# Optimization experiments

Measured on AMD Instinct MI355X. Metric: run time of the kernel, lower is better.

## Reference

```python
import jax, jax.numpy as jnp
import numpy as np

N, M, E, IN, HID = 100000, 2048, 65536, 512, 256
TAU, LAMDA = 0.5, 1.0


def _l2n(a, eps=1e-12):
    # F.normalize: x / max(||x||_2, eps) along dim=1
    return a / jnp.maximum(jnp.linalg.norm(a, axis=1, keepdims=True), eps)


def setup_inputs() -> dict:
    key = jax.random.key(0)
    ks = jax.random.split(key, 16)
    s = 0.05  # weight scale (xavier-like)
    inp = {
        "x": jax.random.normal(ks[0], (N, IN), jnp.float32),
        "We0": jax.random.normal(ks[1], (IN, HID), jnp.float32) * s,
        "be0": jnp.zeros((HID,), jnp.float32),
        "We1": jax.random.normal(ks[2], (HID, HID), jnp.float32) * s,
        "be1": jnp.zeros((HID,), jnp.float32),
        "Wt0": jax.random.normal(ks[3], (IN, HID), jnp.float32) * s,
        "bt0": jnp.zeros((HID,), jnp.float32),
        "Wt1": jax.random.normal(ks[4], (HID, HID), jnp.float32) * s,
        "bt1": jnp.zeros((HID,), jnp.float32),
        "Wp0": jax.random.normal(ks[5], (HID, HID), jnp.float32) * s,
        "bp0": jnp.zeros((HID,), jnp.float32),
        "Wp1": jax.random.normal(ks[6], (HID, HID), jnp.float32) * s,
        "bp1": jnp.zeros((HID,), jnp.float32),
        "p_vals": jnp.ones((N,), jnp.float32),
        "cg_vals": jax.random.uniform(ks[7], (E,), jnp.float32),
        "p_assign": jax.random.randint(ks[8], (N,), 0, M, jnp.int32),
        "cg_rows": jax.random.randint(ks[9], (E,), 0, M, jnp.int32),
        "cg_cols": jax.random.randint(ks[10], (E,), 0, M, jnp.int32),
        "neg_idx": jax.random.randint(ks[11], (N,), 0, M, jnp.int32),
    }
    return inp


def reference(x, We0, be0, We1, be1, Wt0, bt0, Wt1, bt1,
              Wp0, bp0, Wp1, bp1, p_vals, cg_vals,
              p_assign, cg_rows, cg_cols, neg_idx):
    # encoder: stacked Linears, no activation (batch_norm=layer_norm=False)
    h = (x @ We0 + be0) @ We1 + be1                      # [N, HID]
    # h = spmm(P.T, h): per-cluster weighted sum
    hc = jax.ops.segment_sum(p_vals[:, None] * h, p_assign, num_segments=M)  # [M, HID]
    # target encoder
    v = (x @ Wt0 + bt0) @ Wt1 + bt1                      # [N, HID]

    # pos_score: projector (relu between layers, none on last) + normalize
    q = jax.nn.relu(hc @ Wp0 + bp0) @ Wp1 + bp1          # [M, HID]
    q = _l2n(q)
    vn = _l2n(v)
    pos_sim = jnp.sum(vn * q[p_assign], axis=1) / TAU    # [N]
    pos_score = jnp.exp(
        jax.ops.segment_sum(p_vals * pos_sim, p_assign, num_segments=M))[:, None]  # [M,1]

    # neg_score: dense cluster-cluster similarity
    hn = _l2n(hc)
    neg_score = jnp.exp((hn @ hn.T) / TAU)               # [M, M]

    # partition_score = coarse_g @ neg_score (sparse row-scatter)
    partition_score = jax.ops.segment_sum(
        cg_vals[:, None] * neg_score[cg_cols], cg_rows, num_segments=M)  # [M, M]

    loss = jnp.mean(-jnp.log(pos_score + LAMDA * partition_score)
                    + jnp.log(pos_score + neg_score.sum(axis=1)))
    return loss
```

## Files before the change

kernel.cpp:

```cpp
#include <hip/hip_runtime.h>
#include <hip/hip_bf16.h>
#include <math.h>

#define N_PTS  100000
#define M_CL   2048
#define E_EDG  65536
#define IN_DIM 512
#define HID    256

typedef unsigned short u16;
typedef __attribute__((ext_vector_type(8))) short bf16x8;
typedef __attribute__((ext_vector_type(4))) float f32x4;

__device__ __forceinline__ u16 f2bf(float f){
  __hip_bfloat16 h = __float2bfloat16(f);
  return *reinterpret_cast<u16*>(&h);
}
__device__ __forceinline__ unsigned pk2(float a, float b){
  return (unsigned)f2bf(a) | ((unsigned)f2bf(b) << 16);
}
__device__ __forceinline__ float bf2f(u16 v){
  return __uint_as_float((unsigned)v << 16);
}
__device__ __forceinline__ void glds16(const u16* g, u16* lds_base_uniform){
  __builtin_amdgcn_global_load_lds(
      (const __attribute__((address_space(1))) unsigned int*)(g),
      (__attribute__((address_space(3))) unsigned int*)(lds_base_uniform), 16, 0, 0);
}
#define VMWAIT8() do{ asm volatile("s_waitcnt vmcnt(8)" ::: "memory"); __builtin_amdgcn_sched_barrier(0);}while(0)
#define VMWAIT4() do{ asm volatile("s_waitcnt vmcnt(4)" ::: "memory"); __builtin_amdgcn_sched_barrier(0);}while(0)
#define VMWAIT0() do{ asm volatile("s_waitcnt vmcnt(0)" ::: "memory"); __builtin_amdgcn_sched_barrier(0);}while(0)

static const size_t OFF_POSACC = 0;
static const size_t OFF_NEGSUM = 8192;
static const size_t OFF_CURP   = 16384;
static const size_t OFF_CURE   = 24576;
static const size_t OFF_LOSS   = 32768;
static const size_t OFF_DONE   = 32776;
static const size_t OFF_STARTP = 33024;
static const size_t OFF_STARTE = 41472;
static const size_t OFF_SORTPT = 49920;
static const size_t OFF_SCOL   = 450048;
static const size_t OFF_SVAL   = 712192;
static const size_t OFF_CNT    = 974336;
static const size_t OFF_XC     = 982528;
static const size_t OFF_Q      = 9371136;
static const size_t OFF_HNB    = 11468288;
static const size_t OFF_NEGB   = 13565440;
static const size_t OFF_WT0T   = 22020096;
static const size_t OFF_WT1T   = 22282240;
static const size_t OFF_XBF    = 33554432;

__global__ __launch_bounds__(1024) void k_setup(
    const int* __restrict__ pas, const int* __restrict__ cgr,
    int* __restrict__ start_p, int* __restrict__ start_e,
    int* __restrict__ cur_p, int* __restrict__ cur_e,
    float* __restrict__ posacc, float* __restrict__ negsum,
    double* __restrict__ lossd, int* __restrict__ done){
  __shared__ int hist[2048];
  __shared__ int wpart[16];
  const int t = threadIdx.x;
  const int lane = t & 63, wv = t >> 6;

  posacc[2*t] = 0.f; posacc[2*t+1] = 0.f;
  negsum[2*t] = 0.f; negsum[2*t+1] = 0.f;
  cur_p[2*t] = 0;    cur_p[2*t+1] = 0;
  cur_e[2*t] = 0;    cur_e[2*t+1] = 0;
  if (t == 0){ *lossd = 0.0; *done = 0; }
  hist[2*t] = 0; hist[2*t+1] = 0;
  __syncthreads();

  for (int i=t; i<N_PTS; i+=1024) atomicAdd(&hist[pas[i]], 1);
  __syncthreads();
  {
    int v0 = hist[2*t], v1 = hist[2*t+1];
    int s = v0 + v1;
    for (int off=1; off<64; off<<=1){ int n = __shfl_up(s, off, 64); if (lane >= off) s += n; }
    if (lane == 63) wpart[wv] = s;
    __syncthreads();
    if (t == 0){ int run = 0; for (int i=0;i<16;i++){ int tmp = wpart[i]; wpart[i] = run; run += tmp; } }
    __syncthreads();
    int excl = s - (v0+v1) + wpart[wv];
    start_p[2*t] = excl; start_p[2*t+1] = excl + v0;
    if (t == 1023) start_p[2048] = excl + v0 + v1;
  }
  __syncthreads();
  hist[2*t] = 0; hist[2*t+1] = 0;
  __syncthreads();
  for (int i=t; i<E_EDG; i+=1024) atomicAdd(&hist[cgr[i]], 1);
  __syncthreads();
  {
    int v0 = hist[2*t], v1 = hist[2*t+1];
    int s = v0 + v1;
    for (int off=1; off<64; off<<=1){ int n = __shfl_up(s, off, 64); if (lane >= off) s += n; }
    if (lane == 63) wpart[wv] = s;
    __syncthreads();
    if (t == 0){ int run = 0; for (int i=0;i<16;i++){ int tmp = wpart[i]; wpart[i] = run; run += tmp; } }
    __syncthreads();
    int excl = s - (v0+v1) + wpart[wv];
    start_e[2*t] = excl; start_e[2*t+1] = excl + v0;
    if (t == 1023) start_e[2048] = excl + v0 + v1;
  }
}

#define NB_P  ((N_PTS + 255)/256)
#define NB_E  ((E_EDG + 255)/256)
#define NB_T0 ((256*512)/256)
#define NB_T1 ((256*256)/256)
__global__ __launch_bounds__(256) void k_misc(
    const int* __restrict__ pas, const int* __restrict__ cgr, const int* __restrict__ cgc,
    const float* __restrict__ cgv, const int* __restrict__ start_p, const int* __restrict__ start_e,
    int* __restrict__ cur_p, int* __restrict__ cur_e,
    int* __restrict__ sortpt, int* __restrict__ scol, float* __restrict__ sval,
    const float* __restrict__ Wt0, const float* __restrict__ Wt1,
    u16* __restrict__ Wt0t, u16* __restrict__ Wt1t){
  const int b = blockIdx.x, t = threadIdx.x;
  if (b < NB_P){
    int i = b*256 + t;
    if (i < N_PTS){
      int r = pas[i];
      int p = start_p[r] + atomicAdd(&cur_p[r], 1);
      sortpt[p] = i;
    }
  } else if (b < NB_P + NB_E){
    int e = (b - NB_P)*256 + t;
    if (e < E_EDG){
      int r = cgr[e];
      int p = start_e[r] + atomicAdd(&cur_e[r], 1);
      scol[p] = cgc[e];
      sval[p] = cgv[e];
    }
  } else if (b < NB_P + NB_E + NB_T0){
    int o = (b - NB_P - NB_E)*256 + t;
    int n = o / IN_DIM, k = o % IN_DIM;
    Wt0t[o] = f2bf(Wt0[(size_t)k*HID + n]);
  } else {
    int o = (b - NB_P - NB_E - NB_T0)*256 + t;
    int n = o / HID, k = o % HID;
    Wt1t[o] = f2bf(Wt1[(size_t)k*HID + n]);
  }
}

__global__ __launch_bounds__(256) void k_cluster_agg(const float* __restrict__ x, const float* __restrict__ pv,
                                                     const int* __restrict__ sorted_pt, const int* __restrict__ start,
                                                     float* __restrict__ Xc, float* __restrict__ cnt,
                                                     u16* __restrict__ xbf){
  const int m = blockIdx.x;
  const int t = threadIdx.x;
  const int half = t >> 7;
  const int u = t & 127;
  const int s0 = start[m], s1 = start[m+1];
  f32x4 a = {0.f,0.f,0.f,0.f};
  float c = 0.f;
  for (int p = s0 + half; p < s1; p += 2){
    int row = sorted_pt[p];
    float w = pv[row];
    f32x4 xv = *reinterpret_cast<const f32x4*>(x + (size_t)row*IN_DIM + u*4);
    a.x = fmaf(w, xv.x, a.x); a.y = fmaf(w, xv.y, a.y);
    a.z = fmaf(w, xv.z, a.z); a.w = fmaf(w, xv.w, a.w);
    c += w;
    uint2 pk; pk.x = pk2(xv.x, xv.y); pk.y = pk2(xv.z, xv.w);
    *reinterpret_cast<uint2*>(xbf + (size_t)row*IN_DIM + u*4) = pk;
  }
  __shared__ __align__(16) float sh[128*4];
  __shared__ float shc[2];
  if (half == 1) *reinterpret_cast<f32x4*>(sh + u*4) = a;
  if (t == 0)   shc[0] = c;
  if (t == 128) shc[1] = c;
  __syncthreads();
  if (half == 0){
    f32x4 b = *reinterpret_cast<const f32x4*>(sh + u*4);
    a.x += b.x; a.y += b.y; a.z += b.z; a.w += b.w;
    *reinterpret_cast<f32x4*>(Xc + (size_t)m*IN_DIM + u*4) = a;
    if (t == 0) cnt[m] = shc[0] + shc[1];
  }
}

template<int K>
__device__ __forceinline__ void mc_layer(const float* __restrict__ W, const float* act, int t, float acc[4]){
#pragma unroll
  for (int r=0;r<4;r++) acc[r] = 0.f;
#pragma unroll 2
  for (int k=0;k<K;k+=4){
    float w0 = W[(size_t)(k+0)*HID + t];
    float w1 = W[(size_t)(k+1)*HID + t];
    float w2 = W[(size_t)(k+2)*HID + t];
    float w3 = W[(size_t)(k+3)*HID + t];
#pragma unroll
    for (int r=0;r<4;r++){
      float4 av = *reinterpret_cast<const float4*>(act + r*K + k);
      acc[r] = fmaf(av.x, w0, acc[r]);
      acc[r] = fmaf(av.y, w1, acc[r]);
      acc[r] = fmaf(av.z, w2, acc[r]);
      acc[r] = fmaf(av.w, w3, acc[r]);
    }
  }
}

__global__ __launch_bounds__(256) void k_mchain(
    const float* __restrict__ Xc, const float* __restrict__ cnt,
    const float* __restrict__ We0, const float* __restrict__ be0,
    const float* __restrict__ We1, const float* __restrict__ be1,
    const float* __restrict__ Wp0, const float* __restrict__ bp0,
    const float* __restrict__ Wp1, const float* __restrict__ bp1,
    u16* __restrict__ hnb, float* __restrict__ q){
  __shared__ __align__(16) float a_sh[4*512];
  __shared__ __align__(16) float b_sh[4*256];
  __shared__ float part[4][4];
  const int t = threadIdx.x;
  const int rb = blockIdx.x*4;
  for (int i=t; i<4*128; i+=256){
    int r = i>>7, k4 = i&127;
    reinterpret_cast<float4*>(a_sh + r*512)[k4] =
      reinterpret_cast<const float4*>(Xc + (size_t)(rb+r)*IN_DIM)[k4];
  }
  float cv[4];
#pragma unroll
  for (int r=0;r<4;r++) cv[r] = cnt[rb+r];
  __syncthreads();

  float acc[4], v[4];
  mc_layer<512>(We0, a_sh, t, acc);
  {
    float b = be0[t];
#pragma unroll
    for (int r=0;r<4;r++) b_sh[r*256+t] = fmaf(cv[r], b, acc[r]);
  }
  __syncthreads();
  mc_layer<256>(We1, b_sh, t, acc);
  {
    float b = be1[t];
#pragma unroll
    for (int r=0;r<4;r++){
      v[r] = fmaf(cv[r], b, acc[r]);
      float s = v[r]*v[r];
#pragma unroll
      for (int off=32;off;off>>=1) s += __shfl_xor(s, off, 64);
      if ((t&63) == 0) part[t>>6][r] = s;
      a_sh[r*256+t] = v[r];
    }
  }
  __syncthreads();
#pragma unroll
  for (int r=0;r<4;r++){
    float tot = part[0][r]+part[1][r]+part[2][r]+part[3][r];
    float inv = 1.0f / fmaxf(sqrtf(tot), 1e-12f);
    hnb[(size_t)(rb+r)*HID + t] = f2bf(v[r]*inv);
  }
  mc_layer<256>(Wp0, a_sh, t, acc);
  {
    float b = bp0[t];
#pragma unroll
    for (int r=0;r<4;r++) b_sh[r*256+t] = fmaxf(acc[r]+b, 0.f);
  }
  __syncthreads();
  mc_layer<256>(Wp1, b_sh, t, acc);
  {
    float b = bp1[t];
#pragma unroll
    for (int r=0;r<4;r++){
      v[r] = acc[r] + b;
      float s = v[r]*v[r];
#pragma unroll
      for (int off=32;off;off>>=1) s += __shfl_xor(s, off, 64);
      if ((t&63) == 0) part[t>>6][r] = s;
    }
  }
  __syncthreads();
#pragma unroll
  for (int r=0;r<4;r++){
    float tot = part[0][r]+part[1][r]+part[2][r]+part[3][r];
    float inv = 1.0f / fmaxf(sqrtf(tot), 1e-12f);
    q[(size_t)(rb+r)*HID + t] = v[r]*inv;
  }
}

#define NEG_BLKS 256
#define TGT_BLKS ((N_PTS + 63)/64)
__global__ __launch_bounds__(256,2) void k_tneg(
    const u16* __restrict__ xbf, const u16* __restrict__ Wt0t, const float* __restrict__ bt0,
    const u16* __restrict__ Wt1t, const float* __restrict__ bt1,
    const float* __restrict__ q, const int* __restrict__ assign,
    const float* __restrict__ pv, float* __restrict__ posacc,
    const u16* __restrict__ hnb, u16* __restrict__ negb, float* __restrict__ negsum){
  __shared__ u16 wlds[4][2][2048];
  __shared__ u16 act[16384];
  __shared__ float red[2][4][4][16];

  const int t  = threadIdx.x;
  const int w  = t >> 6;
  const int l  = t & 63;
  const int c  = l & 15;
  const int lg = l >> 4;
  const int wrow = l >> 2;
  const int wswz = (l&3) ^ ((wrow>>1)&3);
  const int su = lg ^ ((c>>1)&3);

  f32x4 acc[4][4];
#pragma unroll
  for (int i=0;i<4;i++)
#pragma unroll
    for (int j=0;j<4;j++){ acc[i][j].x=0.f; acc[i][j].y=0.f; acc[i][j].z=0.f; acc[i][j].w=0.f; }

  if (blockIdx.x < NEG_BLKS){
    const int b  = blockIdx.x;
    const int j0 = (b & 7) * 256;
    const int i0 = (b >> 3) * 64;

    #define NSTAGE_W(k0, buf) do { \
      _Pragma("unroll") \
      for (int i_=0;i_<4;i_++){ \
        int row_ = j0 + w*64 + i_*16 + wrow; \
        glds16(hnb + (size_t)row_*HID + (k0) + wswz*8, &wlds[w][buf][i_*512]); \
      } } while(0)

    const u16* irow[4];
#pragma unroll
    for (int mf=0;mf<4;mf++)
      irow[mf] = hnb + (size_t)(i0 + mf*16 + c)*HID + lg*8;

    bf16x8 xreg[2][4];
    NSTAGE_W(0, 0);
#pragma unroll
    for (int mf=0;mf<4;mf++) xreg[0][mf] = *reinterpret_cast<const bf16x8*>(irow[mf]);

#pragma unroll
    for (int ks=0; ks<8; ks++){
      const int buf = ks & 1;
      if (ks < 7){
        NSTAGE_W((ks+1)*32, buf^1);
#pragma unroll
        for (int mf=0;mf<4;mf++)
          xreg[buf^1][mf] = *reinterpret_cast<const bf16x8*>(irow[mf] + (ks+1)*32);
        VMWAIT8();
      } else {
        VMWAIT0();
      }
#pragma unroll
      for (int nf=0; nf<4; nf++){
        bf16x8 afr = *reinterpret_cast<const bf16x8*>(&wlds[w][buf][((nf*16+c)*4 + su)*8]);
#pragma unroll
        for (int mf=0; mf<4; mf++)
          acc[mf][nf] = __builtin_amdgcn_mfma_f32_16x16x32_bf16(afr, xreg[buf][mf], acc[mf][nf], 0,0,0);
      }
    }

#pragma unroll
    for (int mf=0; mf<4; mf++){
      int i = i0 + mf*16 + c;
      float rs = 0.f;
#pragma unroll
      for (int nf=0; nf<4; nf++){
        f32x4 a = acc[mf][nf];
        float e0 = __expf(a.x*2.0f), e1 = __expf(a.y*2.0f);
        float e2 = __expf(a.z*2.0f), e3 = __expf(a.w*2.0f);
        rs += e0+e1+e2+e3;
        uint2 p; p.x = pk2(e0, e1); p.y = pk2(e2, e3);
        *reinterpret_cast<uint2*>(negb + (size_t)i*M_CL + j0 + w*64 + nf*16 + lg*4) = p;
      }
      rs += __shfl_xor(rs, 16, 64); rs += __shfl_xor(rs, 32, 64);
      if (lg == 0) atomicAdd(&negsum[i], rs);
    }
    #undef NSTAGE_W
    return;
  }

  const int gm0 = (blockIdx.x - NEG_BLKS) * 64;

  #define TSTAGE_W(Wt, K, k0, buf) do { \
    _Pragma("unroll") \
    for (int i_=0;i_<4;i_++){ \
      int row_ = w*64 + i_*16 + wrow; \
      glds16((Wt) + (size_t)row_*(K) + (k0) + wswz*8, &wlds[w][buf][i_*512]); \
    } } while(0)

  const u16* xrow[4];
#pragma unroll
  for (int mf=0;mf<4;mf++){
    int gm = gm0 + mf*16 + c; if (gm > N_PTS-1) gm = N_PTS-1;
    xrow[mf] = xbf + (size_t)gm*IN_DIM + lg*8;
  }

  bf16x8 xreg[2][4];
  TSTAGE_W(Wt0t, IN_DIM, 0, 0);
#pragma unroll
  for (int mf=0;mf<4;mf++) xreg[0][mf] = *reinterpret_cast<const bf16x8*>(xrow[mf]);

#pragma unroll
  for (int ks=0; ks<16; ks++){
    const int buf = ks & 1;
    if (ks < 15){
      TSTAGE_W(Wt0t, IN_DIM, (ks+1)*32, buf^1);
#pragma unroll
      for (int mf=0;mf<4;mf++)
        xreg[buf^1][mf] = *reinterpret_cast<const bf16x8*>(xrow[mf] + (ks+1)*32);
      VMWAIT8();
    } else {
      VMWAIT0();
    }
#pragma unroll
    for (int nf=0; nf<4; nf++){
      bf16x8 afr = *reinterpret_cast<const bf16x8*>(&wlds[w][buf][((nf*16+c)*4 + su)*8]);
#pragma unroll
      for (int mf=0; mf<4; mf++)
        acc[mf][nf] = __builtin_amdgcn_mfma_f32_16x16x32_bf16(afr, xreg[buf][mf], acc[mf][nf], 0,0,0);
    }
  }

#pragma unroll
  for (int nf=0; nf<4; nf++){
    f32x4 bias = *reinterpret_cast<const f32x4*>(bt0 + w*64 + nf*16 + lg*4);
#pragma unroll
    for (int mf=0; mf<4; mf++){
      int m = mf*16 + c;
      f32x4 v = acc[mf][nf] + bias;
      uint2 p; p.x = pk2(v.x, v.y); p.y = pk2(v.z, v.w);
      int u = (w*8 + nf*2 + (lg>>1)) ^ (c&7);
      *reinterpret_cast<uint2*>(act + (m*32 + u)*8 + (lg&1)*4) = p;
    }
  }
#pragma unroll
  for (int i=0;i<4;i++)
#pragma unroll
    for (int j=0;j<4;j++){ acc[i][j].x=0.f; acc[i][j].y=0.f; acc[i][j].z=0.f; acc[i][j].w=0.f; }
  __syncthreads();

  TSTAGE_W(Wt1t, HID, 0, 0);
#pragma unroll
  for (int ks=0; ks<8; ks++){
    const int buf = ks & 1;
    if (ks < 7){
      TSTAGE_W(Wt1t, HID, (ks+1)*32, buf^1);
      VMWAIT4();
    } else {
      VMWAIT0();
    }
    bf16x8 bfr[4];
#pragma unroll
    for (int mf=0; mf<4; mf++){
      int m = mf*16 + c;
      int u = (ks*4 + lg) ^ (c&7);
      bfr[mf] = *reinterpret_cast<const bf16x8*>(act + (m*32 + u)*8);
    }
#pragma unroll
    for (int nf=0; nf<4; nf++){
      bf16x8 afr = *reinterpret_cast<const bf16x8*>(&wlds[w][buf][((nf*16+c)*4 + su)*8]);
#pragma unroll
      for (int mf=0; mf<4; mf++)
        acc[mf][nf] = __builtin_amdgcn_mfma_f32_16x16x32_bf16(afr, bfr[mf], acc[mf][nf], 0,0,0);
    }
  }

#pragma unroll
  for (int mf=0; mf<4; mf++){
    int gm = gm0 + mf*16 + c;
    int cl = assign[(gm < N_PTS) ? gm : (N_PTS-1)];
    const float* qrow = q + (size_t)cl*HID + w*64 + lg*4;
    float ss = 0.f, d = 0.f;
#pragma unroll
    for (int nf=0; nf<4; nf++){
      f32x4 b  = *reinterpret_cast<const f32x4*>(bt1 + w*64 + nf*16 + lg*4);
      f32x4 qv = *reinterpret_cast<const f32x4*>(qrow + nf*16);
      f32x4 v  = acc[mf][nf] + b;
      ss = fmaf(v.x,v.x, fmaf(v.y,v.y, fmaf(v.z,v.z, fmaf(v.w,v.w, ss))));
      d  = fmaf(v.x,qv.x, fmaf(v.y,qv.y, fmaf(v.z,qv.z, fmaf(v.w,qv.w, d))));
    }
    ss += __shfl_xor(ss, 16, 64); ss += __shfl_xor(ss, 32, 64);
    d  += __shfl_xor(d , 16, 64); d  += __shfl_xor(d , 32, 64);
    if (lg == 0){ red[0][w][mf][c] = ss; red[1][w][mf][c] = d; }
  }
  __syncthreads();
  if (t < 64){
    int gm = gm0 + t;
    if (gm < N_PTS){
      int mf = t>>4, cc = t&15;
      float ss = red[0][0][mf][cc]+red[0][1][mf][cc]+red[0][2][mf][cc]+red[0][3][mf][cc];
      float d  = red[1][0][mf][cc]+red[1][1][mf][cc]+red[1][2][mf][cc]+red[1][3][mf][cc];
      float inv = 1.0f / fmaxf(sqrtf(ss), 1e-12f);
      atomicAdd(&posacc[assign[gm]], pv[gm] * d * inv * 2.0f);
    }
  }
  #undef TSTAGE_W
}

__global__ __launch_bounds__(256) void k_loss(const u16* __restrict__ negb, const float* __restrict__ negsum,
                                              const float* __restrict__ posacc, const int* __restrict__ start,
                                              const int* __restrict__ scol, const float* __restrict__ sval,
                                              double* __restrict__ lossd, int* __restrict__ done,
                                              float* __restrict__ out){
  const int i = blockIdx.x, t = threadIdx.x;
  float ps[8] = {};
  const int s0 = start[i], s1 = start[i+1];
  for (int e=s0;e<s1;e++){
    int c = scol[e];
    float v = sval[e];
    bf16x8 r = *reinterpret_cast<const bf16x8*>(negb + (size_t)c*M_CL + t*8);
#pragma unroll
    for (int jj=0;jj<8;jj++) ps[jj] = fmaf(v, bf2f((u16)r[jj]), ps[jj]);
  }
  float pos = __expf(posacc[i]);
  f32x4 nsa = *reinterpret_cast<const f32x4*>(negsum + t*8);
  f32x4 nsb = *reinterpret_cast<const f32x4*>(negsum + t*8 + 4);
  float ns[8] = {nsa.x,nsa.y,nsa.z,nsa.w,nsb.x,nsb.y,nsb.z,nsb.w};
  float part = 0.f;
#pragma unroll
  for (int jj=0;jj<8;jj++)
    part += __logf(pos + ns[jj]) - __logf(pos + ps[jj]);
#pragma unroll
  for (int off=32;off;off>>=1) part += __shfl_xor(part, off, 64);
  __shared__ float wsum[4];
  if ((t&63) == 0) wsum[t>>6] = part;
  __syncthreads();
  if (t == 0){
    double s = (double)wsum[0] + (double)wsum[1] + (double)wsum[2] + (double)wsum[3];
    atomicAdd(lossd, s);
    __threadfence();
    int ticket = atomicAdd(done, 1);
    if (ticket == M_CL - 1){
      __threadfence();
      double tot = atomicAdd(lossd, 0.0);
      out[0] = (float)(tot / ((double)M_CL * (double)M_CL));
    }
  }
}

extern "C" void kernel_launch(void* const* d_in, const int* in_sizes, int n_in,
                              void* d_out, int out_size, void* d_ws, size_t ws_size,
                              hipStream_t stream){
  const float* x    = (const float*)d_in[0];
  const float* We0  = (const float*)d_in[1];
  const float* be0  = (const float*)d_in[2];
  const float* We1  = (const float*)d_in[3];
  const float* be1  = (const float*)d_in[4];
  const float* Wt0  = (const float*)d_in[5];
  const float* bt0  = (const float*)d_in[6];
  const float* Wt1  = (const float*)d_in[7];
  const float* bt1  = (const float*)d_in[8];
  const float* Wp0  = (const float*)d_in[9];
  const float* bp0  = (const float*)d_in[10];
  const float* Wp1  = (const float*)d_in[11];
  const float* bp1  = (const float*)d_in[12];
  const float* pv   = (const float*)d_in[13];
  const float* cgv  = (const float*)d_in[14];
  const int*   pas  = (const int*)d_in[15];
  const int*   cgr  = (const int*)d_in[16];
  const int*   cgc  = (const int*)d_in[17];

  char* ws = (char*)d_ws;
  float*  posacc  = (float*)(ws + OFF_POSACC);
  float*  negsum  = (float*)(ws + OFF_NEGSUM);
  int*    cur_p   = (int*)  (ws + OFF_CURP);
  int*    cur_e   = (int*)  (ws + OFF_CURE);
  double* lossd   = (double*)(ws + OFF_LOSS);
  int*    done    = (int*)  (ws + OFF_DONE);
  int*    start_p = (int*)  (ws + OFF_STARTP);
  int*    start_e = (int*)  (ws + OFF_STARTE);
  int*    sortpt  = (int*)  (ws + OFF_SORTPT);
  int*    scol    = (int*)  (ws + OFF_SCOL);
  float*  sval    = (float*)(ws + OFF_SVAL);
  float*  cnt     = (float*)(ws + OFF_CNT);
  float*  Xc      = (float*)(ws + OFF_XC);
  float*  qb      = (float*)(ws + OFF_Q);
  u16*    hnb     = (u16*)  (ws + OFF_HNB);
  u16*    negb    = (u16*)  (ws + OFF_NEGB);
  u16*    Wt0t    = (u16*)  (ws + OFF_WT0T);
  u16*    Wt1t    = (u16*)  (ws + OFF_WT1T);
  u16*    xbf     = (u16*)  (ws + OFF_XBF);

  k_setup<<<1, 1024, 0, stream>>>(pas, cgr, start_p, start_e, cur_p, cur_e,
                                  posacc, negsum, lossd, done);

  k_misc<<<NB_P + NB_E + NB_T0 + NB_T1, 256, 0, stream>>>(
      pas, cgr, cgc, cgv, start_p, start_e, cur_p, cur_e,
      sortpt, scol, sval, Wt0, Wt1, Wt0t, Wt1t);

  k_cluster_agg<<<M_CL, 256, 0, stream>>>(x, pv, sortpt, start_p, Xc, cnt, xbf);

  k_mchain<<<M_CL/4, 256, 0, stream>>>(Xc, cnt, We0, be0, We1, be1, Wp0, bp0, Wp1, bp1, hnb, qb);

  k_tneg<<<NEG_BLKS + TGT_BLKS, 256, 0, stream>>>(
      xbf, Wt0t, bt0, Wt1t, bt1, qb, pas, pv, posacc, hnb, negb, negsum);

  k_loss<<<M_CL, 256, 0, stream>>>(negb, negsum, posacc, start_e, scol, sval, lossd, done, (float*)d_out);
}
```

Before: 397.9 us.

## Split target-encoder GEMM chain into weight-stationary persistent kernels and parallelize setup

Replaces the single-block setup kernel with a parallel zeroing kernel, a multi-block histogram kernel and a small scan kernel. Splits the fused target-encoder/negative-score kernel into a separate neg-similarity kernel and three target kernels: a persistent first-layer GEMM that keeps its weight slice resident in LDS and writes a bf16 intermediate to global memory, a persistent second-layer GEMM fused with the dot/norm epilogue writing per-half partials, and a final reduction kernel. The aim is to stop reloading weights per row tile and to remove the serial single-block setup, at the cost of an extra global round-trip for the hidden activations and more kernel launches.

```diff
diff --git a/kernel.cpp b/kernel.cpp
--- a/kernel.cpp
+++ b/kernel.cpp
@@ -27,80 +27,77 @@
       (const __attribute__((address_space(1))) unsigned int*)(g),
       (__attribute__((address_space(3))) unsigned int*)(lds_base_uniform), 16, 0, 0);
 }
+#define VMWAIT0() do{ asm volatile("s_waitcnt vmcnt(0)" ::: "memory"); __builtin_amdgcn_sched_barrier(0);}while(0)
 #define VMWAIT8() do{ asm volatile("s_waitcnt vmcnt(8)" ::: "memory"); __builtin_amdgcn_sched_barrier(0);}while(0)
-#define VMWAIT4() do{ asm volatile("s_waitcnt vmcnt(4)" ::: "memory"); __builtin_amdgcn_sched_barrier(0);}while(0)
-#define VMWAIT0() do{ asm volatile("s_waitcnt vmcnt(0)" ::: "memory"); __builtin_amdgcn_sched_barrier(0);}while(0)
 
 static const size_t OFF_POSACC = 0;
 static const size_t OFF_NEGSUM = 8192;
 static const size_t OFF_CURP   = 16384;
 static const size_t OFF_CURE   = 24576;
-static const size_t OFF_LOSS   = 32768;
-static const size_t OFF_DONE   = 32776;
-static const size_t OFF_STARTP = 33024;
-static const size_t OFF_STARTE = 41472;
-static const size_t OFF_SORTPT = 49920;
-static const size_t OFF_SCOL   = 450048;
-static const size_t OFF_SVAL   = 712192;
-static const size_t OFF_CNT    = 974336;
-static const size_t OFF_XC     = 982528;
-static const size_t OFF_Q      = 9371136;
-static const size_t OFF_HNB    = 11468288;
-static const size_t OFF_NEGB   = 13565440;
-static const size_t OFF_WT0T   = 22020096;
-static const size_t OFF_WT1T   = 22282240;
+static const size_t OFF_HISTP  = 32768;
+static const size_t OFF_HISTE  = 40960;
+static const size_t OFF_LOSS   = 49152;
+static const size_t OFF_DONE   = 49160;
+static const int    ZERO_U32   = 12291;
+static const size_t OFF_STARTP = 49664;
+static const size_t OFF_STARTE = 58368;
+static const size_t OFF_SORTPT = 66816;
+static const size_t OFF_SCOL   = 466944;
+static const size_t OFF_SVAL   = 729088;
+static const size_t OFF_CNT    = 991232;
+static const size_t OFF_XC     = 999424;
+static const size_t OFF_Q      = 5193728;
+static const size_t OFF_HNB    = 7290880;
+static const size_t OFF_NEGB   = 8388608;
+static const size_t OFF_WT0T   = 16777216;
+static const size_t OFF_WT1T   = 17039360;
 static const size_t OFF_XBF    = 33554432;
-
-__global__ __launch_bounds__(1024) void k_setup(
-    const int* __restrict__ pas, const int* __restrict__ cgr,
-    int* __restrict__ start_p, int* __restrict__ start_e,
-    int* __restrict__ cur_p, int* __restrict__ cur_e,
-    float* __restrict__ posacc, float* __restrict__ negsum,
-    double* __restrict__ lossd, int* __restrict__ done){
-  __shared__ int hist[2048];
-  __shared__ int wpart[16];
+static const size_t OFF_TBUF   = 150994944;
+static const size_t OFF_PSS    = 260046848;
+static const size_t OFF_PD     = 268435456;
+
+__global__ __launch_bounds__(256) void k_pre0(unsigned* __restrict__ p){
+  int i = blockIdx.x*256 + threadIdx.x;
+  if (i < ZERO_U32) p[i] = 0u;
+}
+
+#define NB_HP ((N_PTS + 255)/256)
+#define NB_HE ((E_EDG + 255)/256)
+__global__ __launch_bounds__(256) void k_hist(const int* __restrict__ pas, const int* __restrict__ cgr,
+                                              int* __restrict__ hist_p, int* __restrict__ hist_e){
+  const int b = blockIdx.x, t = threadIdx.x;
+  if (b < NB_HP){
+    int i = b*256 + t;
+    if (i < N_PTS) atomicAdd(&hist_p[pas[i]], 1);
+  } else {
+    int e = (b - NB_HP)*256 + t;
+    if (e < E_EDG) atomicAdd(&hist_e[cgr[e]], 1);
+  }
+}
+
+__device__ __forceinline__ void scan8(const int* __restrict__ hist, int* __restrict__ start, int* part){
   const int t = threadIdx.x;
-  const int lane = t & 63, wv = t >> 6;
-
-  posacc[2*t] = 0.f; posacc[2*t+1] = 0.f;
-  negsum[2*t] = 0.f; negsum[2*t+1] = 0.f;
-  cur_p[2*t] = 0;    cur_p[2*t+1] = 0;
-  cur_e[2*t] = 0;    cur_e[2*t+1] = 0;
-  if (t == 0){ *lossd = 0.0; *done = 0; }
-  hist[2*t] = 0; hist[2*t+1] = 0;
-  __syncthreads();
-
-  for (int i=t; i<N_PTS; i+=1024) atomicAdd(&hist[pas[i]], 1);
-  __syncthreads();
-  {
-    int v0 = hist[2*t], v1 = hist[2*t+1];
-    int s = v0 + v1;
-    for (int off=1; off<64; off<<=1){ int n = __shfl_up(s, off, 64); if (lane >= off) s += n; }
-    if (lane == 63) wpart[wv] = s;
-    __syncthreads();
-    if (t == 0){ int run = 0; for (int i=0;i<16;i++){ int tmp = wpart[i]; wpart[i] = run; run += tmp; } }
-    __syncthreads();
-    int excl = s - (v0+v1) + wpart[wv];
-    start_p[2*t] = excl; start_p[2*t+1] = excl + v0;
-    if (t == 1023) start_p[2048] = excl + v0 + v1;
-  }
-  __syncthreads();
-  hist[2*t] = 0; hist[2*t+1] = 0;
-  __syncthreads();
-  for (int i=t; i<E_EDG; i+=1024) atomicAdd(&hist[cgr[i]], 1);
-  __syncthreads();
-  {
-    int v0 = hist[2*t], v1 = hist[2*t+1];
-    int s = v0 + v1;
-    for (int off=1; off<64; off<<=1){ int n = __shfl_up(s, off, 64); if (lane >= off) s += n; }
-    if (lane == 63) wpart[wv] = s;
-    __syncthreads();
-    if (t == 0){ int run = 0; for (int i=0;i<16;i++){ int tmp = wpart[i]; wpart[i] = run; run += tmp; } }
-    __syncthreads();
-    int excl = s - (v0+v1) + wpart[wv];
-    start_e[2*t] = excl; start_e[2*t+1] = excl + v0;
-    if (t == 1023) start_e[2048] = excl + v0 + v1;
-  }
+  int v[8]; int s = 0;
+#pragma unroll
+  for (int j=0;j<8;j++){ v[j] = hist[t*8+j]; s += v[j]; }
+  part[t] = s;
+  __syncthreads();
+  if (t == 0){
+    int run = 0;
+    for (int i=0;i<256;i++){ int tmp = part[i]; part[i] = run; run += tmp; }
+  }
+  __syncthreads();
+  int run = part[t];
+#pragma unroll
+  for (int j=0;j<8;j++){ start[t*8+j] = run; run += v[j]; }
+  if (t == 255) start[M_CL] = run;
+}
+__global__ __launch_bounds__(256) void k_scan2(const int* __restrict__ hp, int* __restrict__ sp,
+                                               const int* __restrict__ he, int* __restrict__ se){
+  __shared__ int part[256];
+  scan8(hp, sp, part);
+  __syncthreads();
+  scan8(he, se, part);
 }
 
 #define NB_P  ((N_PTS + 255)/256)
@@ -275,125 +272,212 @@
   }
 }
 
-#define NEG_BLKS 256
-#define TGT_BLKS ((N_PTS + 63)/64)
-__global__ __launch_bounds__(256,2) void k_tneg(
+#define NT0_TILES ((N_PTS + 255)/256)
+__global__ __launch_bounds__(512,2) void k_t0(
     const u16* __restrict__ xbf, const u16* __restrict__ Wt0t, const float* __restrict__ bt0,
-    const u16* __restrict__ Wt1t, const float* __restrict__ bt1,
-    const float* __restrict__ q, const int* __restrict__ assign,
-    const float* __restrict__ pv, float* __restrict__ posacc,
-    const u16* __restrict__ hnb, u16* __restrict__ negb, float* __restrict__ negsum){
-  __shared__ u16 wlds[4][2][2048];
-  __shared__ u16 act[16384];
-  __shared__ float red[2][4][4][16];
-
+    u16* __restrict__ tbuf){
+  __shared__ u16 wbuf[16*64*32];
   const int t  = threadIdx.x;
   const int w  = t >> 6;
   const int l  = t & 63;
   const int c  = l & 15;
   const int lg = l >> 4;
+  const int nq   = blockIdx.x & 3;
+  const int pair = blockIdx.x >> 2;
+  const int nbase = nq*64;
+
+  {
+#pragma unroll
+    for (int kk=0; kk<2; kk++){
+      const int ks = 2*w + kk;
+#pragma unroll
+      for (int i_=0; i_<4; i_++){
+        int row = i_*16 + (l>>2);
+        int ug  = (l&3) ^ ((row>>1)&3);
+        glds16(Wt0t + (size_t)(nbase + row)*IN_DIM + ks*32 + ug*8,
+               wbuf + ks*2048 + i_*512);
+      }
+    }
+  }
+  VMWAIT0();
+  __syncthreads();
+
+  const int su = lg ^ ((c>>1)&3);
+
+  for (int tile = pair; tile < NT0_TILES; tile += 64){
+    const int m0 = tile*256 + w*32;
+    int g0 = m0 + c;      if (g0 > N_PTS-1) g0 = N_PTS-1;
+    int g1 = m0 + 16 + c; if (g1 > N_PTS-1) g1 = N_PTS-1;
+    const u16* xr0 = xbf + (size_t)g0*IN_DIM + lg*8;
+    const u16* xr1 = xbf + (size_t)g1*IN_DIM + lg*8;
+
+    f32x4 acc[2][4];
+#pragma unroll
+    for (int i=0;i<2;i++)
+#pragma unroll
+      for (int j=0;j<4;j++){ acc[i][j].x=0.f; acc[i][j].y=0.f; acc[i][j].z=0.f; acc[i][j].w=0.f; }
+
+    bf16x8 xa = *reinterpret_cast<const bf16x8*>(xr0);
+    bf16x8 xb = *reinterpret_cast<const bf16x8*>(xr1);
+#pragma unroll
+    for (int ks=0; ks<16; ks++){
+      bf16x8 cxa = xa, cxb = xb;
+      if (ks < 15){
+        xa = *reinterpret_cast<const bf16x8*>(xr0 + (ks+1)*32);
+        xb = *reinterpret_cast<const bf16x8*>(xr1 + (ks+1)*32);
+      }
+#pragma unroll
+      for (int nf=0; nf<4; nf++){
+        bf16x8 afr = *reinterpret_cast<const bf16x8*>(wbuf + ks*2048 + (nf*16+c)*32 + su*8);
+        acc[0][nf] = __builtin_amdgcn_mfma_f32_16x16x32_bf16(afr, cxa, acc[0][nf], 0,0,0);
+        acc[1][nf] = __builtin_amdgcn_mfma_f32_16x16x32_bf16(afr, cxb, acc[1][nf], 0,0,0);
+      }
+    }
+
+#pragma unroll
+    for (int nf=0; nf<4; nf++){
+      f32x4 b = *reinterpret_cast<const f32x4*>(bt0 + nbase + nf*16 + lg*4);
+#pragma unroll
+      for (int mf=0; mf<2; mf++){
+        int m = m0 + mf*16 + c;
+        f32x4 v = acc[mf][nf] + b;
+        uint2 p; p.x = pk2(v.x, v.y); p.y = pk2(v.z, v.w);
+        *reinterpret_cast<uint2*>(tbuf + (size_t)m*HID + nbase + nf*16 + lg*4) = p;
+      }
+    }
+  }
+}
+
+#define NT1_TILES ((N_PTS + 127)/128)
+__global__ __launch_bounds__(512,2) void k_t1(
+    const u16* __restrict__ tbuf, const u16* __restrict__ Wt1t, const float* __restrict__ bt1,
+    const float* __restrict__ q, const int* __restrict__ assign,
+    float* __restrict__ pss, float* __restrict__ pd){
+  __shared__ u16 wbuf[8*128*32];
+  const int t  = threadIdx.x;
+  const int w  = t >> 6;
+  const int l  = t & 63;
+  const int c  = l & 15;
+  const int lg = l >> 4;
+  const int half = blockIdx.x & 1;
+  const int pair = blockIdx.x >> 1;
+  const int nbase = half*128;
+
+  {
+    const int ks = w;
+#pragma unroll
+    for (int i_=0; i_<8; i_++){
+      int row = i_*16 + (l>>2);
+      int ug  = (l&3) ^ ((row>>1)&3);
+      glds16(Wt1t + (size_t)(nbase + row)*HID + ks*32 + ug*8,
+             wbuf + ks*4096 + i_*512);
+    }
+  }
+  VMWAIT0();
+  __syncthreads();
+
+  const int su = lg ^ ((c>>1)&3);
+
+  for (int tile = pair; tile < NT1_TILES; tile += 128){
+    const int gm = tile*128 + w*16 + c;
+    const int gmc = (gm < N_PTS) ? gm : (N_PTS-1);
+    const u16* trow = tbuf + (size_t)gmc*HID + lg*8;
+
+    f32x4 acc[8];
+#pragma unroll
+    for (int j=0;j<8;j++){ acc[j].x=0.f; acc[j].y=0.f; acc[j].z=0.f; acc[j].w=0.f; }
+
+    bf16x8 xa = *reinterpret_cast<const bf16x8*>(trow);
+#pragma unroll
+    for (int ks=0; ks<8; ks++){
+      bf16x8 cxa = xa;
+      if (ks < 7) xa = *reinterpret_cast<const bf16x8*>(trow + (ks+1)*32);
+#pragma unroll
+      for (int nf=0; nf<8; nf++){
+        bf16x8 afr = *reinterpret_cast<const bf16x8*>(wbuf + ks*4096 + (nf*16+c)*32 + su*8);
+        acc[nf] = __builtin_amdgcn_mfma_f32_16x16x32_bf16(afr, cxa, acc[nf], 0,0,0);
+      }
+    }
+
+    const int cl = assign[gmc];
+    const float* qrow = q + (size_t)cl*HID + nbase + lg*4;
+    float ss = 0.f, d = 0.f;
+#pragma unroll
+    for (int nf=0; nf<8; nf++){
+      f32x4 b  = *reinterpret_cast<const f32x4*>(bt1 + nbase + nf*16 + lg*4);
+      f32x4 qv = *reinterpret_cast<const f32x4*>(qrow + nf*16);
+      f32x4 v  = acc[nf] + b;
+      ss = fmaf(v.x,v.x, fmaf(v.y,v.y, fmaf(v.z,v.z, fmaf(v.w,v.w, ss))));
+      d  = fmaf(v.x,qv.x, fmaf(v.y,qv.y, fmaf(v.z,qv.z, fmaf(v.w,qv.w, d))));
+    }
+    ss += __shfl_xor(ss, 16, 64); ss += __shfl_xor(ss, 32, 64);
+    d  += __shfl_xor(d , 16, 64); d  += __shfl_xor(d , 32, 64);
+    if (lg == 0 && gm < N_PTS){
+      pss[(size_t)gm*2 + half] = ss;
+      pd [(size_t)gm*2 + half] = d;
+    }
+  }
+}
+
+__global__ __launch_bounds__(256) void k_t2(const float* __restrict__ pss, const float* __restrict__ pd,
+                                            const int* __restrict__ assign, const float* __restrict__ pv,
+                                            float* __restrict__ posacc){
+  int i = blockIdx.x*256 + threadIdx.x;
+  if (i < N_PTS){
+    float ss = pss[2*i] + pss[2*i+1];
+    float d  = pd[2*i]  + pd[2*i+1];
+    float inv = 1.0f / fmaxf(sqrtf(ss), 1e-12f);
+    atomicAdd(&posacc[assign[i]], pv[i] * d * inv * 2.0f);
+  }
+}
+
+__global__ __launch_bounds__(256) void k_neg_mfma(
+    const u16* __restrict__ hnb, u16* __restrict__ negb, float* __restrict__ negsum){
+  __shared__ u16 wlds[4][2][2048];
+  const int t  = threadIdx.x;
+  const int w  = t >> 6;
+  const int l  = t & 63;
+  const int c  = l & 15;
+  const int lg = l >> 4;
+  const int j0 = blockIdx.x * 256;
+  const int i0 = blockIdx.y * 64;
+
   const int wrow = l >> 2;
   const int wswz = (l&3) ^ ((wrow>>1)&3);
-  const int su = lg ^ ((c>>1)&3);
-
-  f32x4 acc[4][4];
-#pragma unroll
-  for (int i=0;i<4;i++)
-#pragma unroll
-    for (int j=0;j<4;j++){ acc[i][j].x=0.f; acc[i][j].y=0.f; acc[i][j].z=0.f; acc[i][j].w=0.f; }
-
-  if (blockIdx.x < NEG_BLKS){
-    const int b  = blockIdx.x;
-    const int j0 = (b & 7) * 256;
-    const int i0 = (b >> 3) * 64;
-
-    #define NSTAGE_W(k0, buf) do { \
-      _Pragma("unroll") \
-      for (int i_=0;i_<4;i_++){ \
-        int row_ = j0 + w*64 + i_*16 + wrow; \
-        glds16(hnb + (size_t)row_*HID + (k0) + wswz*8, &wlds[w][buf][i_*512]); \
-      } } while(0)
-
-    const u16* irow[4];
-#pragma unroll
-    for (int mf=0;mf<4;mf++)
-      irow[mf] = hnb + (size_t)(i0 + mf*16 + c)*HID + lg*8;
-
-    bf16x8 xreg[2][4];
-    NSTAGE_W(0, 0);
-#pragma unroll
-    for (int mf=0;mf<4;mf++) xreg[0][mf] = *reinterpret_cast<const bf16x8*>(irow[mf]);
-
-#pragma unroll
-    for (int ks=0; ks<8; ks++){
-      const int buf = ks & 1;
-      if (ks < 7){
-        NSTAGE_W((ks+1)*32, buf^1);
-#pragma unroll
-        for (int mf=0;mf<4;mf++)
-          xreg[buf^1][mf] = *reinterpret_cast<const bf16x8*>(irow[mf] + (ks+1)*32);
-        VMWAIT8();
-      } else {
-        VMWAIT0();
-      }
-#pragma unroll
-      for (int nf=0; nf<4; nf++){
-        bf16x8 afr = *reinterpret_cast<const bf16x8*>(&wlds[w][buf][((nf*16+c)*4 + su)*8]);
-#pragma unroll
-        for (int mf=0; mf<4; mf++)
-          acc[mf][nf] = __builtin_amdgcn_mfma_f32_16x16x32_bf16(afr, xreg[buf][mf], acc[mf][nf], 0,0,0);
-      }
-    }
-
-#pragma unroll
-    for (int mf=0; mf<4; mf++){
-      int i = i0 + mf*16 + c;
-      float rs = 0.f;
-#pragma unroll
-      for (int nf=0; nf<4; nf++){
-        f32x4 a = acc[mf][nf];
-        float e0 = __expf(a.x*2.0f), e1 = __expf(a.y*2.0f);
-        float e2 = __expf(a.z*2.0f), e3 = __expf(a.w*2.0f);
-        rs += e0+e1+e2+e3;
-        uint2 p; p.x = pk2(e0, e1); p.y = pk2(e2, e3);
-        *reinterpret_cast<uint2*>(negb + (size_t)i*M_CL + j0 + w*64 + nf*16 + lg*4) = p;
-      }
-      rs += __shfl_xor(rs, 16, 64); rs += __shfl_xor(rs, 32, 64);
-      if (lg == 0) atomicAdd(&negsum[i], rs);
-    }
-    #undef NSTAGE_W
-    return;
-  }
-
-  const int gm0 = (blockIdx.x - NEG_BLKS) * 64;
-
-  #define TSTAGE_W(Wt, K, k0, buf) do { \
+
+  #define NSTAGE_W(k0, buf) do { \
     _Pragma("unroll") \
     for (int i_=0;i_<4;i_++){ \
-      int row_ = w*64 + i_*16 + wrow; \
-      glds16((Wt) + (size_t)row_*(K) + (k0) + wswz*8, &wlds[w][buf][i_*512]); \
+      int row_ = j0 + w*64 + i_*16 + wrow; \
+      glds16(hnb + (size_t)row_*HID + (k0) + wswz*8, &wlds[w][buf][i_*512]); \
     } } while(0)
 
-  const u16* xrow[4];
-#pragma unroll
-  for (int mf=0;mf<4;mf++){
-    int gm = gm0 + mf*16 + c; if (gm > N_PTS-1) gm = N_PTS-1;
-    xrow[mf] = xbf + (size_t)gm*IN_DIM + lg*8;
-  }
+  const u16* irow[4];
+#pragma unroll
+  for (int mf=0;mf<4;mf++)
+    irow[mf] = hnb + (size_t)(i0 + mf*16 + c)*HID + lg*8;
+
+  f32x4 acc[4][4];
+#pragma unroll
+  for (int i=0;i<4;i++)
+#pragma unroll
+    for (int j=0;j<4;j++){ acc[i][j].x=0.f; acc[i][j].y=0.f; acc[i][j].z=0.f; acc[i][j].w=0.f; }
+
+  const int su = lg ^ ((c>>1)&3);
 
   bf16x8 xreg[2][4];
-  TSTAGE_W(Wt0t, IN_DIM, 0, 0);
-#pragma unroll
-  for (int mf=0;mf<4;mf++) xreg[0][mf] = *reinterpret_cast<const bf16x8*>(xrow[mf]);
-
-#pragma unroll
-  for (int ks=0; ks<16; ks++){
+  NSTAGE_W(0, 0);
+#pragma unroll
+  for (int mf=0;mf<4;mf++) xreg[0][mf] = *reinterpret_cast<const bf16x8*>(irow[mf]);
+
+#pragma unroll
+  for (int ks=0; ks<8; ks++){
     const int buf = ks & 1;
-    if (ks < 15){
-      TSTAGE_W(Wt0t, IN_DIM, (ks+1)*32, buf^1);
+    if (ks < 7){
+      NSTAGE_W((ks+1)*32, buf^1);
 #pragma unroll
       for (int mf=0;mf<4;mf++)
-        xreg[buf^1][mf] = *reinterpret_cast<const bf16x8*>(xrow[mf] + (ks+1)*32);
+        xreg[buf^1][mf] = *reinterpret_cast<const bf16x8*>(irow[mf] + (ks+1)*32);
       VMWAIT8();
     } else {
       VMWAIT0();
@@ -408,79 +492,22 @@
   }
 
 #pragma unroll
-  for (int nf=0; nf<4; nf++){
-    f32x4 bias = *reinterpret_cast<const f32x4*>(bt0 + w*64 + nf*16 + lg*4);
-#pragma unroll
-    for (int mf=0; mf<4; mf++){
-      int m = mf*16 + c;
-      f32x4 v = acc[mf][nf] + bias;
-      uint2 p; p.x = pk2(v.x, v.y); p.y = pk2(v.z, v.w);
-      int u = (w*8 + nf*2 + (lg>>1)) ^ (c&7);
-      *reinterpret_cast<uint2*>(act + (m*32 + u)*8 + (lg&1)*4) = p;
-    }
-  }
-#pragma unroll
-  for (int i=0;i<4;i++)
-#pragma unroll
-    for (int j=0;j<4;j++){ acc[i][j].x=0.f; acc[i][j].y=0.f; acc[i][j].z=0.f; acc[i][j].w=0.f; }
-  __syncthreads();
-
-  TSTAGE_W(Wt1t, HID, 0, 0);
-#pragma unroll
-  for (int ks=0; ks<8; ks++){
-    const int buf = ks & 1;
-    if (ks < 7){
-      TSTAGE_W(Wt1t, HID, (ks+1)*32, buf^1);
-      VMWAIT4();
-    } else {
-      VMWAIT0();
-    }
-    bf16x8 bfr[4];
-#pragma unroll
-    for (int mf=0; mf<4; mf++){
-      int m = mf*16 + c;
-      int u = (ks*4 + lg) ^ (c&7);
-      bfr[mf] = *reinterpret_cast<const bf16x8*>(act + (m*32 + u)*8);
-    }
+  for (int mf=0; mf<4; mf++){
+    int i = i0 + mf*16 + c;
+    float rs = 0.f;
 #pragma unroll
     for (int nf=0; nf<4; nf++){
-      bf16x8 afr = *reinterpret_cast<const bf16x8*>(&wlds[w][buf][((nf*16+c)*4 + su)*8]);
-#pragma unroll
-      for (int mf=0; mf<4; mf++)
-        acc[mf][nf] = __builtin_amdgcn_mfma_f32_16x16x32_bf16(afr, bfr[mf], acc[mf][nf], 0,0,0);
-    }
-  }
-
-#pragma unroll
-  for (int mf=0; mf<4; mf++){
-    int gm = gm0 + mf*16 + c;
-    int cl = assign[(gm < N_PTS) ? gm : (N_PTS-1)];
-    const float* qrow = q + (size_t)cl*HID + w*64 + lg*4;
-    float ss = 0.f, d = 0.f;
-#pragma unroll
-    for (int nf=0; nf<4; nf++){
-      f32x4 b  = *reinterpret_cast<const f32x4*>(bt1 + w*64 + nf*16 + lg*4);
-      f32x4 qv = *reinterpret_cast<const f32x4*>(qrow + nf*16);
-      f32x4 v  = acc[mf][nf] + b;
-      ss = fmaf(v.x,v.x, fmaf(v.y,v.y, fmaf(v.z,v.z, fmaf(v.w,v.w, ss))));
-      d  = fmaf(v.x,qv.x, fmaf(v.y,qv.y, fmaf(v.z,qv.z, fmaf(v.w,qv.w, d))));
-    }
-    ss += __shfl_xor(ss, 16, 64); ss += __shfl_xor(ss, 32, 64);
-    d  += __shfl_xor(d , 16, 64); d  += __shfl_xor(d , 32, 64);
-    if (lg == 0){ red[0][w][mf][c] = ss; red[1][w][mf][c] = d; }
-  }
-  __syncthreads();
-  if (t < 64){
-    int gm = gm0 + t;
-    if (gm < N_PTS){
-      int mf = t>>4, cc = t&15;
-      float ss = red[0][0][mf][cc]+red[0][1][mf][cc]+red[0][2][mf][cc]+red[0][3][mf][cc];
-      float d  = red[1][0][mf][cc]+red[1][1][mf][cc]+red[1][2][mf][cc]+red[1][3][mf][cc];
-      float inv = 1.0f / fmaxf(sqrtf(ss), 1e-12f);
-      atomicAdd(&posacc[assign[gm]], pv[gm] * d * inv * 2.0f);
-    }
-  }
-  #undef TSTAGE_W
+      f32x4 a = acc[mf][nf];
+      float e0 = __expf(a.x*2.0f), e1 = __expf(a.y*2.0f);
+      float e2 = __expf(a.z*2.0f), e3 = __expf(a.w*2.0f);
+      rs += e0+e1+e2+e3;
+      uint2 p; p.x = pk2(e0, e1); p.y = pk2(e2, e3);
+      *reinterpret_cast<uint2*>(negb + (size_t)i*M_CL + j0 + w*64 + nf*16 + lg*4) = p;
+    }
+    rs += __shfl_xor(rs, 16, 64); rs += __shfl_xor(rs, 32, 64);
+    if (lg == 0) atomicAdd(&negsum[i], rs);
+  }
+  #undef NSTAGE_W
 }
 
 __global__ __launch_bounds__(256) void k_loss(const u16* __restrict__ negb, const float* __restrict__ negsum,
@@ -551,6 +578,8 @@
   float*  negsum  = (float*)(ws + OFF_NEGSUM);
   int*    cur_p   = (int*)  (ws + OFF_CURP);
   int*    cur_e   = (int*)  (ws + OFF_CURE);
+  int*    hist_p  = (int*)  (ws + OFF_HISTP);
+  int*    hist_e  = (int*)  (ws + OFF_HISTE);
   double* lossd   = (double*)(ws + OFF_LOSS);
   int*    done    = (int*)  (ws + OFF_DONE);
   int*    start_p = (int*)  (ws + OFF_STARTP);
@@ -566,10 +595,13 @@
   u16*    Wt0t    = (u16*)  (ws + OFF_WT0T);
   u16*    Wt1t    = (u16*)  (ws + OFF_WT1T);
   u16*    xbf     = (u16*)  (ws + OFF_XBF);
-
-  k_setup<<<1, 1024, 0, stream>>>(pas, cgr, start_p, start_e, cur_p, cur_e,
-                                  posacc, negsum, lossd, done);
-
+  u16*    tbuf    = (u16*)  (ws + OFF_TBUF);
+  float*  pss     = (float*)(ws + OFF_PSS);
+  float*  pd      = (float*)(ws + OFF_PD);
+
+  k_pre0<<<(ZERO_U32 + 255)/256, 256, 0, stream>>>((unsigned*)ws);
+  k_hist<<<NB_HP + NB_HE, 256, 0, stream>>>(pas, cgr, hist_p, hist_e);
+  k_scan2<<<1, 256, 0, stream>>>(hist_p, start_p, hist_e, start_e);
   k_misc<<<NB_P + NB_E + NB_T0 + NB_T1, 256, 0, stream>>>(
       pas, cgr, cgc, cgv, start_p, start_e, cur_p, cur_e,
       sortpt, scol, sval, Wt0, Wt1, Wt0t, Wt1t);
@@ -578,8 +610,12 @@
 
   k_mchain<<<M_CL/4, 256, 0, stream>>>(Xc, cnt, We0, be0, We1, be1, Wp0, bp0, Wp1, bp1, hnb, qb);
 
-  k_tneg<<<NEG_BLKS + TGT_BLKS, 256, 0, stream>>>(
-      xbf, Wt0t, bt0, Wt1t, bt1, qb, pas, pv, posacc, hnb, negb, negsum);
+  dim3 gneg(M_CL/256, M_CL/64);
+  k_neg_mfma<<<gneg, 256, 0, stream>>>(hnb, negb, negsum);
+
+  k_t0<<<256, 512, 0, stream>>>(xbf, Wt0t, bt0, tbuf);
+  k_t1<<<256, 512, 0, stream>>>(tbuf, Wt1t, bt1, qb, pas, pss, pd);
+  k_t2<<<(N_PTS + 255)/256, 256, 0, stream>>>(pss, pd, pas, pv, posacc);
 
   k_loss<<<M_CL, 256, 0, stream>>>(negb, negsum, posacc, start_e, scol, sval, lossd, done, (float*)d_out);
 }
```

Result: slower. 546.2 us (+37.3%).

## Parallelize setup histograms across blocks and split prefix scan into separate kernel

Applied to the files above, without the earlier changes.

Replaces the single-block setup kernel with two kernels. A multi-block init kernel zeroes the accumulator and counter region and builds both cluster and edge histograms in global memory with atomics. A small one-block kernel then scans both histograms, 8 entries per thread, to produce the start offsets. The goal is to remove the serial cost of one 1024-thread block looping over all 100k points and 65k edges; the trade-offs are an extra launch, global atomics, and the workspace offsets being repacked. Zeroing the histogram region and atomically incrementing it in the same grid depends on the zero blocks running before the histogram blocks, which is not guaranteed.

```diff
diff --git a/kernel.cpp b/kernel.cpp
--- a/kernel.cpp
+++ b/kernel.cpp
@@ -27,80 +27,75 @@
       (const __attribute__((address_space(1))) unsigned int*)(g),
       (__attribute__((address_space(3))) unsigned int*)(lds_base_uniform), 16, 0, 0);
 }
+#define VMWAIT0() do{ asm volatile("s_waitcnt vmcnt(0)" ::: "memory"); __builtin_amdgcn_sched_barrier(0);}while(0)
+#define VMWAIT4() do{ asm volatile("s_waitcnt vmcnt(4)" ::: "memory"); __builtin_amdgcn_sched_barrier(0);}while(0)
 #define VMWAIT8() do{ asm volatile("s_waitcnt vmcnt(8)" ::: "memory"); __builtin_amdgcn_sched_barrier(0);}while(0)
-#define VMWAIT4() do{ asm volatile("s_waitcnt vmcnt(4)" ::: "memory"); __builtin_amdgcn_sched_barrier(0);}while(0)
-#define VMWAIT0() do{ asm volatile("s_waitcnt vmcnt(0)" ::: "memory"); __builtin_amdgcn_sched_barrier(0);}while(0)
 
 static const size_t OFF_POSACC = 0;
 static const size_t OFF_NEGSUM = 8192;
 static const size_t OFF_CURP   = 16384;
 static const size_t OFF_CURE   = 24576;
-static const size_t OFF_LOSS   = 32768;
-static const size_t OFF_DONE   = 32776;
-static const size_t OFF_STARTP = 33024;
-static const size_t OFF_STARTE = 41472;
-static const size_t OFF_SORTPT = 49920;
-static const size_t OFF_SCOL   = 450048;
-static const size_t OFF_SVAL   = 712192;
-static const size_t OFF_CNT    = 974336;
-static const size_t OFF_XC     = 982528;
-static const size_t OFF_Q      = 9371136;
-static const size_t OFF_HNB    = 11468288;
-static const size_t OFF_NEGB   = 13565440;
-static const size_t OFF_WT0T   = 22020096;
-static const size_t OFF_WT1T   = 22282240;
+static const size_t OFF_HISTP  = 32768;
+static const size_t OFF_HISTE  = 40960;
+static const size_t OFF_LOSS   = 49152;
+static const size_t OFF_DONE   = 49160;
+static const int    ZERO_U32   = 12291;
+static const size_t OFF_STARTP = 49664;
+static const size_t OFF_STARTE = 58368;
+static const size_t OFF_SORTPT = 66816;
+static const size_t OFF_SCOL   = 466944;
+static const size_t OFF_SVAL   = 729088;
+static const size_t OFF_CNT    = 991232;
+static const size_t OFF_XC     = 999424;
+static const size_t OFF_Q      = 5193728;
+static const size_t OFF_HNB    = 7290880;
+static const size_t OFF_NEGB   = 8388608;
+static const size_t OFF_WT0T   = 16777216;
+static const size_t OFF_WT1T   = 17039360;
 static const size_t OFF_XBF    = 33554432;
 
-__global__ __launch_bounds__(1024) void k_setup(
-    const int* __restrict__ pas, const int* __restrict__ cgr,
-    int* __restrict__ start_p, int* __restrict__ start_e,
-    int* __restrict__ cur_p, int* __restrict__ cur_e,
-    float* __restrict__ posacc, float* __restrict__ negsum,
-    double* __restrict__ lossd, int* __restrict__ done){
-  __shared__ int hist[2048];
-  __shared__ int wpart[16];
+#define NB_Z  ((ZERO_U32 + 255)/256)
+#define NB_HP ((N_PTS + 255)/256)
+#define NB_HE ((E_EDG + 255)/256)
+__global__ __launch_bounds__(256) void k_init(unsigned* __restrict__ zreg,
+                                              const int* __restrict__ pas, const int* __restrict__ cgr,
+                                              int* __restrict__ hist_p, int* __restrict__ hist_e){
+  const int b = blockIdx.x, t = threadIdx.x;
+  if (b < NB_Z){
+    int i = b*256 + t;
+    if (i < ZERO_U32) zreg[i] = 0u;
+  } else if (b < NB_Z + NB_HP){
+    int i = (b - NB_Z)*256 + t;
+    if (i < N_PTS) atomicAdd(&hist_p[pas[i]], 1);
+  } else {
+    int e = (b - NB_Z - NB_HP)*256 + t;
+    if (e < E_EDG) atomicAdd(&hist_e[cgr[e]], 1);
+  }
+}
+
+__device__ __forceinline__ void scan8(const int* __restrict__ hist, int* __restrict__ start, int* part){
   const int t = threadIdx.x;
-  const int lane = t & 63, wv = t >> 6;
-
-  posacc[2*t] = 0.f; posacc[2*t+1] = 0.f;
-  negsum[2*t] = 0.f; negsum[2*t+1] = 0.f;
-  cur_p[2*t] = 0;    cur_p[2*t+1] = 0;
-  cur_e[2*t] = 0;    cur_e[2*t+1] = 0;
-  if (t == 0){ *lossd = 0.0; *done = 0; }
-  hist[2*t] = 0; hist[2*t+1] = 0;
-  __syncthreads();
-
-  for (int i=t; i<N_PTS; i+=1024) atomicAdd(&hist[pas[i]], 1);
-  __syncthreads();
-  {
-    int v0 = hist[2*t], v1 = hist[2*t+1];
-    int s = v0 + v1;
-    for (int off=1; off<64; off<<=1){ int n = __shfl_up(s, off, 64); if (lane >= off) s += n; }
-    if (lane == 63) wpart[wv] = s;
-    __syncthreads();
-    if (t == 0){ int run = 0; for (int i=0;i<16;i++){ int tmp = wpart[i]; wpart[i] = run; run += tmp; } }
-    __syncthreads();
-    int excl = s - (v0+v1) + wpart[wv];
-    start_p[2*t] = excl; start_p[2*t+1] = excl + v0;
-    if (t == 1023) start_p[2048] = excl + v0 + v1;
-  }
-  __syncthreads();
-  hist[2*t] = 0; hist[2*t+1] = 0;
-  __syncthreads();
-  for (int i=t; i<E_EDG; i+=1024) atomicAdd(&hist[cgr[i]], 1);
-  __syncthreads();
-  {
-    int v0 = hist[2*t], v1 = hist[2*t+1];
-    int s = v0 + v1;
-    for (int off=1; off<64; off<<=1){ int n = __shfl_up(s, off, 64); if (lane >= off) s += n; }
-    if (lane == 63) wpart[wv] = s;
-    __syncthreads();
-    if (t == 0){ int run = 0; for (int i=0;i<16;i++){ int tmp = wpart[i]; wpart[i] = run; run += tmp; } }
-    __syncthreads();
-    int excl = s - (v0+v1) + wpart[wv];
-    start_e[2*t] = excl; start_e[2*t+1] = excl + v0;
-    if (t == 1023) start_e[2048] = excl + v0 + v1;
-  }
+  int v[8]; int s = 0;
+#pragma unroll
+  for (int j=0;j<8;j++){ v[j] = hist[t*8+j]; s += v[j]; }
+  part[t] = s;
+  __syncthreads();
+  if (t == 0){
+    int run = 0;
+    for (int i=0;i<256;i++){ int tmp = part[i]; part[i] = run; run += tmp; }
+  }
+  __syncthreads();
+  int run = part[t];
+#pragma unroll
+  for (int j=0;j<8;j++){ start[t*8+j] = run; run += v[j]; }
+  if (t == 255) start[M_CL] = run;
+}
+__global__ __launch_bounds__(256) void k_scan2(const int* __restrict__ hp, int* __restrict__ sp,
+                                               const int* __restrict__ he, int* __restrict__ se){
+  __shared__ int part[256];
+  scan8(hp, sp, part);
+  __syncthreads();
+  scan8(he, se, part);
 }
 
 #define NB_P  ((N_PTS + 255)/256)
@@ -551,6 +546,8 @@
   float*  negsum  = (float*)(ws + OFF_NEGSUM);
   int*    cur_p   = (int*)  (ws + OFF_CURP);
   int*    cur_e   = (int*)  (ws + OFF_CURE);
+  int*    hist_p  = (int*)  (ws + OFF_HISTP);
+  int*    hist_e  = (int*)  (ws + OFF_HISTE);
   double* lossd   = (double*)(ws + OFF_LOSS);
   int*    done    = (int*)  (ws + OFF_DONE);
   int*    start_p = (int*)  (ws + OFF_STARTP);
@@ -567,9 +564,8 @@
   u16*    Wt1t    = (u16*)  (ws + OFF_WT1T);
   u16*    xbf     = (u16*)  (ws + OFF_XBF);
 
-  k_setup<<<1, 1024, 0, stream>>>(pas, cgr, start_p, start_e, cur_p, cur_e,
-                                  posacc, negsum, lossd, done);
-
+  k_init<<<NB_Z + NB_HP + NB_HE, 256, 0, stream>>>((unsigned*)ws, pas, cgr, hist_p, hist_e);
+  k_scan2<<<1, 256, 0, stream>>>(hist_p, start_p, hist_e, start_e);
   k_misc<<<NB_P + NB_E + NB_T0 + NB_T1, 256, 0, stream>>>(
       pas, cgr, cgc, cgv, start_p, start_e, cur_p, cur_e,
       sortpt, scol, sval, Wt0, Wt1, Wt0t, Wt1t);
```

Measured after the change: 357.4 us. -10.2%, faster.
